# Performance work log

Measured on AMD Instinct MI355X. Metric: run time of the kernel, lower is better.

## Reference

```python
import jax, jax.numpy as jnp
import numpy as np

B1, B2, R, L, D, H = 48, 48, 36, 30, 1024, 4
EPS = 1e-8


def _l2norm(x):
    return x / (jnp.sqrt(jnp.sum(x * x, axis=-1, keepdims=True)) + EPS)


def _summary_attn(x, w1, b1, w2, b2):
    # x: (B1,B2,N,D). MLP scores -> softmax over N -> weighted mean over H heads.
    h = jax.nn.relu(jnp.einsum('abnd,ed->abne', x, w1) + b1)
    s = jnp.einsum('abne,he->abnh', h, w2) + b2          # (B1,B2,N,H)
    p = jax.nn.softmax(jnp.swapaxes(s, -1, -2), axis=-1)  # (B1,B2,H,N)
    w = jnp.einsum('abhn,abnd->abhd', p, x)               # (B1,B2,H,D)
    return w.mean(axis=-2)                                # (B1,B2,D)


def setup_inputs() -> dict:
    key = jax.random.key(0)
    ks = jax.random.split(key, 12)
    r = np.sqrt(6.0) / np.sqrt(D + D)  # xavier uniform as in init_weights
    return {
        'v1': jax.random.normal(ks[0], (B1, R, D), dtype=jnp.float32),
        'v2': jax.random.normal(ks[1], (B2, L, D), dtype=jnp.float32),
        'w_img': jax.random.uniform(ks[2], (D, D), jnp.float32, -r, r),
        'w_txt': jax.random.uniform(ks[3], (D, D), jnp.float32, -r, r),
        'w1a': jax.random.normal(ks[4], (D, D), jnp.float32) * 0.02,
        'b1a': jnp.zeros((D,), jnp.float32),
        'w2a': jax.random.normal(ks[5], (H, D), jnp.float32) * 0.02,
        'b2a': jnp.zeros((H,), jnp.float32),
        'w1b': jax.random.normal(ks[6], (D, D), jnp.float32) * 0.02,
        'b1b': jnp.zeros((D,), jnp.float32),
        'w2b': jax.random.normal(ks[7], (H, D), jnp.float32) * 0.02,
        'b2b': jnp.zeros((H,), jnp.float32),
    }


def reference(v1, v2, w_img, w_txt, w1a, b1a, w2a, b2a, w1b, b1b, w2b, b2b):
    d = v1.shape[-1]
    inv_sqrt_d = np.float32(1.0 / np.sqrt(d))
    k1 = jnp.einsum('ard,ed->are', v1, w_img)  # (B1,R,D)
    k2 = jnp.einsum('bld,ed->ble', v2, w_txt)  # (B2,L,D)

    # qkv_attention(k2, k1, v1): queries=words, keys/values=regions
    s1 = jnp.einsum('bld,ard->ablr', k2, k1) * inv_sqrt_d   # (B1,B2,L,R)
    p1 = jax.nn.softmax(s1, axis=-1)
    fused_v2 = jnp.einsum('ablr,ard->abld', p1, v1)         # weighted_v1 -> fused_v2

    # qkv_attention(k1, k2, v2): queries=regions, keys/values=words
    s2 = jnp.einsum('ard,bld->abrl', k1, k2) * inv_sqrt_d   # (B1,B2,R,L)
    p2 = jax.nn.softmax(s2, axis=-1)
    fused_v1 = jnp.einsum('abrl,bld->abrd', p2, v2)         # weighted_v2 -> fused_v1

    co_v1 = _l2norm(_summary_attn(fused_v1, w1a, b1a, w2a, b2a))
    co_v2 = _l2norm(_summary_attn(fused_v2, w1b, b1b, w2b, b2b))
    return jnp.sum(co_v1 * co_v2, axis=-1)  # (B1,B2) score matrix
```

## Files before the change

kernel.cpp:

```cpp
#include <hip/hip_runtime.h>

#define D 1024
#define NB1 48
#define NB2 48
#define RR 36
#define LL 30
#define NH 4

typedef short bf16x8 __attribute__((ext_vector_type(8)));
typedef float f32x4 __attribute__((ext_vector_type(4)));
typedef float f32x2 __attribute__((ext_vector_type(2)));
typedef unsigned short u16x8 __attribute__((ext_vector_type(8)));

#define MFMA16(a, b, c) __builtin_amdgcn_mfma_f32_16x16x32_bf16(a, b, c, 0, 0, 0)

__device__ __forceinline__ unsigned short f2bf(float x) {
  unsigned u = __float_as_uint(x);
  u += 0x7FFF + ((u >> 16) & 1);
  return (unsigned short)(u >> 16);
}
__device__ __forceinline__ float bf2f(unsigned short h) {
  return __uint_as_float(((unsigned)h) << 16);
}
__device__ __forceinline__ void split8(const float* v, bf16x8& h8, bf16x8& l8) {
  u16x8 hi, lo;
#pragma unroll
  for (int i = 0; i < 8; ++i) {
    unsigned short h = f2bf(v[i]);
    hi[i] = h;
    lo[i] = f2bf(v[i] - bf2f(h));
  }
  h8 = __builtin_bit_cast(bf16x8, hi);
  l8 = __builtin_bit_cast(bf16x8, lo);
}
__device__ __forceinline__ f32x2 shflx2(f32x2 v, int m) {
  double d = __builtin_bit_cast(double, v);
  d = __shfl_xor(d, m);
  return __builtin_bit_cast(f32x2, d);
}

__device__ __forceinline__ void conv_body(const float* __restrict__ X,
                                          unsigned short* __restrict__ out,
                                          int rows, int g) {
  const int lane = threadIdx.x & 63;
  const int tile = g >> 5, kc = g & 31;
  const int row = tile * 16 + (lane & 15);
  const int k = kc * 32 + (lane >> 4) * 8;
  float v[8];
  if (row < rows) {
    const float4* s = (const float4*)(X + (size_t)row * 1024 + k);
    float4 x0 = s[0], x1 = s[1];
    v[0] = x0.x; v[1] = x0.y; v[2] = x0.z; v[3] = x0.w;
    v[4] = x1.x; v[5] = x1.y; v[6] = x1.z; v[7] = x1.w;
  } else {
#pragma unroll
    for (int i = 0; i < 8; ++i) v[i] = 0.f;
  }
  bf16x8 hi, lo;
  split8(v, hi, lo);
  bf16x8* o = (bf16x8*)(out + (size_t)g * 1024 + lane * 8);
  o[0] = hi;
  o[64] = lo;
}

__global__ __launch_bounds__(256) void conv6(
    const float* __restrict__ v1, const float* __restrict__ v2,
    const float* __restrict__ wimg, const float* __restrict__ wtxt,
    const float* __restrict__ w1a, const float* __restrict__ w1b,
    unsigned short* v1f, unsigned short* v2f, unsigned short* wimgf,
    unsigned short* wtxtf, unsigned short* w1af, unsigned short* w1bf) {
  const float* X; unsigned short* O; int rows;
  switch (blockIdx.y) {
    case 0: X = v1; O = v1f; rows = 1728; break;
    case 1: X = v2; O = v2f; rows = 1440; break;
    case 2: X = wimg; O = wimgf; rows = 1024; break;
    case 3: X = wtxt; O = wtxtf; rows = 1024; break;
    case 4: X = w1a; O = w1af; rows = 1024; break;
    default: X = w1b; O = w1bf; rows = 1024; break;
  }
  const int tiles = (rows + 15) >> 4;
  const int g = blockIdx.x * 4 + (threadIdx.x >> 6);
  if (g >= tiles * 32) return;
  conv_body(X, O, rows, g);
}

__global__ __launch_bounds__(256) void conv_k(const float* __restrict__ k1,
                                              const float* __restrict__ k2,
                                              unsigned short* k1f, unsigned short* k2f) {
  const float* X = blockIdx.y ? k2 : k1;
  unsigned short* O = blockIdx.y ? k2f : k1f;
  const int rows = blockIdx.y ? 1440 : 1728;
  const int tiles = (rows + 15) >> 4;
  const int g = blockIdx.x * 4 + (threadIdx.x >> 6);
  if (g >= tiles * 32) return;
  conv_body(X, O, rows, g);
}

__global__ __launch_bounds__(256) void convG(const float* __restrict__ G2a,
                                             const float* __restrict__ G1b,
                                             const float* __restrict__ w2a,
                                             const float* __restrict__ w2b,
                                             unsigned short* G2aF, unsigned short* G1bF,
                                             float4* __restrict__ w2at,
                                             float4* __restrict__ w2bt) {
  const int t = threadIdx.x, lane = t & 63;
  if (blockIdx.y == 0 && blockIdx.x < 4) {
    int col = blockIdx.x * 256 + t;
    w2at[col] = make_float4(w2a[col], w2a[1024 + col], w2a[2048 + col], w2a[3072 + col]);
    w2bt[col] = make_float4(w2b[col], w2b[1024 + col], w2b[2048 + col], w2b[3072 + col]);
  }
  const int bb = blockIdx.x >> 4;
  const int nt = ((blockIdx.x & 15) << 2) + (t >> 6);
  const int c = lane & 15, q = lane >> 4;
  if (blockIdx.y == 0) {
    float v[8];
#pragma unroll
    for (int j = 0; j < 8; ++j) {
      int l = q * 8 + j;
      v[j] = (l < LL) ? G2a[(size_t)(bb * LL + l) * D + nt * 16 + c] : 0.f;
    }
    bf16x8 hi, lo;
    split8(v, hi, lo);
    bf16x8* o = (bf16x8*)(G2aF + ((size_t)(bb * 64 + nt) * 2) * 512 + lane * 8);
    o[0] = hi;
    o[64] = lo;
  } else {
#pragma unroll
    for (int kc = 0; kc < 2; ++kc) {
      float v[8];
#pragma unroll
      for (int j = 0; j < 8; ++j) {
        int r = kc * 32 + q * 8 + j;
        v[j] = (r < RR) ? G1b[(size_t)(bb * RR + r) * D + nt * 16 + c] : 0.f;
      }
      bf16x8 hi, lo;
      split8(v, hi, lo);
      bf16x8* o = (bf16x8*)(G1bF + (((size_t)(bb * 64 + nt) * 2 + kc) * 2) * 512 + lane * 8);
      o[0] = hi;
      o[64] = lo;
    }
  }
}

#define LOAD_FRAGS(AH, AL, BH, BL)                                              \
  {                                                                             \
    _Pragma("unroll") for (int i = 0; i < 4; ++i) {                             \
      AH[i] = Af[ab[i]]; AL[i] = Af[ab[i] + 64]; ab[i] += 128;                  \
    }                                                                           \
    _Pragma("unroll") for (int j = 0; j < 4; ++j) {                             \
      BH[j] = Bf[bb[j]]; BL[j] = Bf[bb[j] + 64]; bb[j] += 128;                  \
    }                                                                           \
  }

#define MFMA_SET(AH, AL, BH, BL)                                                \
  _Pragma("unroll") for (int i = 0; i < 4; ++i)                                 \
      _Pragma("unroll") for (int j = 0; j < 4; ++j) {                           \
    acc[i][j] = MFMA16(AH[i], BH[j], acc[i][j]);                                \
    acc[i][j] = MFMA16(AL[i], BH[j], acc[i][j]);                                \
    acc[i][j] = MFMA16(AH[i], BL[j], acc[i][j]);                                \
  }

__device__ __forceinline__ void gemm4_body(const bf16x8* __restrict__ Af,
                                           const bf16x8* __restrict__ Bf,
                                           float* __restrict__ C,
                                           int M, int N, float scale,
                                           int Mtiles, int Ntiles) {
  const int lane = threadIdx.x & 63;
  const int w = threadIdx.x >> 6;
  const int mb = blockIdx.y * 8 + (w >> 1) * 4;
  const int nb = blockIdx.x * 8 + (w & 1) * 4;
  int ab[4], bb[4];
#pragma unroll
  for (int i = 0; i < 4; ++i) {
    int tm = mb + i; if (tm > Mtiles - 1) tm = Mtiles - 1;
    ab[i] = tm * 4096 + lane;
    int tn = nb + i; if (tn > Ntiles - 1) tn = Ntiles - 1;
    bb[i] = tn * 4096 + lane;
  }
  f32x4 acc[4][4];
#pragma unroll
  for (int i = 0; i < 4; ++i)
#pragma unroll
    for (int j = 0; j < 4; ++j) acc[i][j] = (f32x4){0.f, 0.f, 0.f, 0.f};

  bf16x8 ahA[4], alA[4], bhA[4], blA[4];
  bf16x8 ahB[4], alB[4], bhB[4], blB[4];
  LOAD_FRAGS(ahA, alA, bhA, blA);
#pragma unroll 1
  for (int kc = 0; kc < 30; kc += 2) {
    LOAD_FRAGS(ahB, alB, bhB, blB);
    MFMA_SET(ahA, alA, bhA, blA);
    LOAD_FRAGS(ahA, alA, bhA, blA);
    MFMA_SET(ahB, alB, bhB, blB);
  }
  LOAD_FRAGS(ahB, alB, bhB, blB);
  MFMA_SET(ahA, alA, bhA, blA);
  MFMA_SET(ahB, alB, bhB, blB);

  const int c16 = lane & 15, q = lane >> 4;
#pragma unroll
  for (int i = 0; i < 4; ++i) {
#pragma unroll
    for (int reg = 0; reg < 4; ++reg) {
      int r = (mb + i) * 16 + q * 4 + reg;
      if (r < M) {
#pragma unroll
        for (int j = 0; j < 4; ++j) {
          int col = (nb + j) * 16 + c16;
          if (col < N) C[(size_t)r * N + col] = acc[i][j][reg] * scale;
        }
      }
    }
  }
}

__global__ __launch_bounds__(256) void proj_fused(
    const bf16x8* __restrict__ v1f, const bf16x8* __restrict__ v2f,
    const bf16x8* __restrict__ wimgf, const bf16x8* __restrict__ wtxtf,
    const bf16x8* __restrict__ w1af, const bf16x8* __restrict__ w1bf,
    float* k1, float* k2, float* G2a, float* G1b) {
  const int z = blockIdx.z;
  const bf16x8* Af = (z == 0 || z == 3) ? v1f : v2f;
  const bf16x8* Bf = (z == 0) ? wimgf : (z == 1) ? wtxtf : (z == 2) ? w1af : w1bf;
  float* C = (z == 0) ? k1 : (z == 1) ? k2 : (z == 2) ? G2a : G1b;
  const int M = (z == 0 || z == 3) ? 1728 : 1440;
  const int Mt = (z == 0 || z == 3) ? 108 : 92;
  if ((int)blockIdx.y * 8 >= Mt) return;
  gemm4_body(Af, Bf, C, M, 1024, 1.f, Mt, 64);
}

__global__ __launch_bounds__(256) void cross_s(
    const bf16x8* __restrict__ k2f, const bf16x8* __restrict__ k1f,
    float* Sbuf) {
  gemm4_body(k2f, k1f, Sbuf, 1440, 1728, 0.03125f, 92, 108);
}

__global__ __launch_bounds__(256, 4) void pair_dir(
    const float* __restrict__ Sb,
    const bf16x8* __restrict__ G2aF, const bf16x8* __restrict__ G1bF,
    const float* __restrict__ b1a, const float4* __restrict__ w2at, const float* __restrict__ b2a,
    const float* __restrict__ b1b, const float4* __restrict__ w2bt, const float* __restrict__ b2b,
    float* __restrict__ U1buf, float* __restrict__ U2buf) {
  const int t = threadIdx.x, lane = t & 63, w = t >> 6;
  const int id = blockIdx.x * 4 + w;
  const int pair = id >> 1, dir = id & 1;
  const int a = pair / NB2;
  const int b = pair - a * NB2;
  const int c16 = lane & 15, q = lane >> 4;

  union WSM {
    struct { float p2s[48][36]; float sa[48][NH]; float qa[48]; } A;
    struct { float p1s[32][68]; float sbm[32][NH]; float qb[32]; } B;
  };
  __shared__ __align__(16) WSM sm[4];
  WSM& S = sm[w];

  const float* Sab = Sb + (size_t)(b * LL) * 1728 + a * RR;

  if (dir == 0) {
    for (int i = lane; i < 48 * 36; i += 64) ((float*)S.A.p2s)[i] = 0.f;
    __builtin_amdgcn_sched_barrier(0);
    for (int i = lane; i < LL * RR; i += 64) {
      int l = i / RR, r = i - l * RR;
      S.A.p2s[r][l] = Sab[(size_t)l * 1728 + r];
    }
    __builtin_amdgcn_sched_barrier(0);
    if (lane < RR) {
      const int r = lane;
      float m = -1e30f;
      for (int l = 0; l < LL; ++l) m = fmaxf(m, S.A.p2s[r][l]);
      float s = 0.f;
      for (int l = 0; l < LL; ++l) {
        float e = __expf(S.A.p2s[r][l] - m);
        S.A.p2s[r][l] = e;
        s += e;
      }
      float inv = 1.f / s;
      for (int l = 0; l < LL; ++l) S.A.p2s[r][l] *= inv;
    }
    __builtin_amdgcn_sched_barrier(0);

    bf16x8 pAh[3], pAl[3];
#pragma unroll
    for (int mt = 0; mt < 3; ++mt) {
      float v[8];
      const float* rp = &S.A.p2s[mt * 16 + c16][q * 8];
      float4 x0 = *(const float4*)rp;
      float4 x1 = *(const float4*)(rp + 4);
      v[0] = x0.x; v[1] = x0.y; v[2] = x0.z; v[3] = x0.w;
      v[4] = x1.x; v[5] = x1.y; v[6] = x1.z; v[7] = x1.w;
      split8(v, pAh[mt], pAl[mt]);
    }

    f32x2 sc01[3][4], sc23[3][4];
#pragma unroll
    for (int mt = 0; mt < 3; ++mt)
#pragma unroll
      for (int reg = 0; reg < 4; ++reg) {
        sc01[mt][reg] = (f32x2){0.f, 0.f};
        sc23[mt][reg] = (f32x2){0.f, 0.f};
      }

    const bf16x8* gA = G2aF + (size_t)(b * 64) * 128 + lane;
#pragma unroll 2
    for (int it = 0; it < 64; ++it) {
      const bf16x8* gp = gA + (size_t)it * 128;
      bf16x8 Bh = gp[0], Bl = gp[64];
      const int col = it * 16 + c16;
      float4 wv = w2at[col];
      float bias = b1a[col];
      f32x2 w01 = {wv.x, wv.y}, w23 = {wv.z, wv.w};
#pragma unroll
      for (int mt = 0; mt < 3; ++mt) {
        f32x4 acc = {bias, bias, bias, bias};
        __builtin_amdgcn_s_setprio(1);
        acc = MFMA16(pAh[mt], Bh, acc);
        acc = MFMA16(pAl[mt], Bh, acc);
        acc = MFMA16(pAh[mt], Bl, acc);
        __builtin_amdgcn_s_setprio(0);
#pragma unroll
        for (int reg = 0; reg < 4; ++reg) {
          float hv = fmaxf(acc[reg], 0.f);
          f32x2 hv2 = {hv, hv};
          sc01[mt][reg] += hv2 * w01;
          sc23[mt][reg] += hv2 * w23;
        }
      }
    }
    f32x2 b01 = {b2a[0], b2a[1]}, b23 = {b2a[2], b2a[3]};
#pragma unroll
    for (int mt = 0; mt < 3; ++mt)
#pragma unroll
      for (int reg = 0; reg < 4; ++reg) {
        f32x2 v01 = sc01[mt][reg], v23 = sc23[mt][reg];
#pragma unroll
        for (int m = 1; m <= 8; m <<= 1) {
          v01 += shflx2(v01, m);
          v23 += shflx2(v23, m);
        }
        if (c16 == 0) {
          f32x2* rp = (f32x2*)&S.A.sa[mt * 16 + q * 4 + reg][0];
          rp[0] = v01 + b01;
          rp[1] = v23 + b23;
        }
      }
    __builtin_amdgcn_sched_barrier(0);
    {
      const int h = q, i = c16;
      float x0 = S.A.sa[i][h];
      float x1 = S.A.sa[i + 16][h];
      float x2 = (i < 4) ? S.A.sa[i + 32][h] : -1e30f;
      float m = fmaxf(fmaxf(x0, x1), x2);
      m = fmaxf(m, __shfl_xor(m, 1));
      m = fmaxf(m, __shfl_xor(m, 2));
      m = fmaxf(m, __shfl_xor(m, 4));
      m = fmaxf(m, __shfl_xor(m, 8));
      float e0 = __expf(x0 - m), e1 = __expf(x1 - m);
      float e2 = (i < 4) ? __expf(x2 - m) : 0.f;
      float s = e0 + e1 + e2;
      s += __shfl_xor(s, 1);
      s += __shfl_xor(s, 2);
      s += __shfl_xor(s, 4);
      s += __shfl_xor(s, 8);
      float inv = 0.25f / s;
      float p0 = e0 * inv, p1 = e1 * inv, p2v = e2 * inv;
      p0 += __shfl_xor(p0, 16); p0 += __shfl_xor(p0, 32);
      p1 += __shfl_xor(p1, 16); p1 += __shfl_xor(p1, 32);
      p2v += __shfl_xor(p2v, 16); p2v += __shfl_xor(p2v, 32);
      if (q == 0) {
        S.A.qa[i] = p0;
        S.A.qa[i + 16] = p1;
        if (i < 4) S.A.qa[i + 32] = p2v;
      }
    }
    __builtin_amdgcn_sched_barrier(0);
    if (lane < LL) {
      const int l = lane;
      float x = 0.f;
      for (int r = 0; r < RR; ++r) x = fmaf(S.A.qa[r], S.A.p2s[r][l], x);
      U2buf[((size_t)b * 48 + a) * 32 + l] = x;
    }
  } else {
    for (int i = lane; i < 32 * 68; i += 64) ((float*)S.B.p1s)[i] = 0.f;
    __builtin_amdgcn_sched_barrier(0);
    for (int i = lane; i < LL * RR; i += 64) {
      int l = i / RR, r = i - l * RR;
      S.B.p1s[l][r] = Sab[(size_t)l * 1728 + r];
    }
    __builtin_amdgcn_sched_barrier(0);
    if (lane < LL) {
      const int l = lane;
      float m = -1e30f;
      for (int r = 0; r < RR; ++r) m = fmaxf(m, S.B.p1s[l][r]);
      float s = 0.f;
      for (int r = 0; r < RR; ++r) {
        float e = __expf(S.B.p1s[l][r] - m);
        S.B.p1s[l][r] = e;
        s += e;
      }
      float inv = 1.f / s;
      for (int r = 0; r < RR; ++r) S.B.p1s[l][r] *= inv;
    }
    __builtin_amdgcn_sched_barrier(0);

    bf16x8 pBh[2][2], pBl[2][2];
#pragma unroll
    for (int mt = 0; mt < 2; ++mt)
#pragma unroll
      for (int kc = 0; kc < 2; ++kc) {
        float v[8];
        const float* rp = &S.B.p1s[mt * 16 + c16][kc * 32 + q * 8];
        float4 x0 = *(const float4*)rp;
        float4 x1 = *(const float4*)(rp + 4);
        v[0] = x0.x; v[1] = x0.y; v[2] = x0.z; v[3] = x0.w;
        v[4] = x1.x; v[5] = x1.y; v[6] = x1.z; v[7] = x1.w;
        split8(v, pBh[mt][kc], pBl[mt][kc]);
      }

    f32x2 sc01[2][4], sc23[2][4];
#pragma unroll
    for (int mt = 0; mt < 2; ++mt)
#pragma unroll
      for (int reg = 0; reg < 4; ++reg) {
        sc01[mt][reg] = (f32x2){0.f, 0.f};
        sc23[mt][reg] = (f32x2){0.f, 0.f};
      }

    const bf16x8* gB = G1bF + (size_t)(a * 64) * 256 + lane;
#pragma unroll 2
    for (int it = 0; it < 64; ++it) {
      const bf16x8* gp = gB + (size_t)it * 256;
      bf16x8 B0h = gp[0], B0l = gp[64], B1h = gp[128], B1l = gp[192];
      const int col = it * 16 + c16;
      float4 wv = w2bt[col];
      float bias = b1b[col];
      f32x2 w01 = {wv.x, wv.y}, w23 = {wv.z, wv.w};
#pragma unroll
      for (int mt = 0; mt < 2; ++mt) {
        f32x4 acc = {bias, bias, bias, bias};
        __builtin_amdgcn_s_setprio(1);
        acc = MFMA16(pBh[mt][0], B0h, acc);
        acc = MFMA16(pBl[mt][0], B0h, acc);
        acc = MFMA16(pBh[mt][0], B0l, acc);
        acc = MFMA16(pBh[mt][1], B1h, acc);
        acc = MFMA16(pBl[mt][1], B1h, acc);
        acc = MFMA16(pBh[mt][1], B1l, acc);
        __builtin_amdgcn_s_setprio(0);
#pragma unroll
        for (int reg = 0; reg < 4; ++reg) {
          float hv = fmaxf(acc[reg], 0.f);
          f32x2 hv2 = {hv, hv};
          sc01[mt][reg] += hv2 * w01;
          sc23[mt][reg] += hv2 * w23;
        }
      }
    }
    f32x2 b01 = {b2b[0], b2b[1]}, b23 = {b2b[2], b2b[3]};
#pragma unroll
    for (int mt = 0; mt < 2; ++mt)
#pragma unroll
      for (int reg = 0; reg < 4; ++reg) {
        f32x2 v01 = sc01[mt][reg], v23 = sc23[mt][reg];
#pragma unroll
        for (int m = 1; m <= 8; m <<= 1) {
          v01 += shflx2(v01, m);
          v23 += shflx2(v23, m);
        }
        if (c16 == 0) {
          f32x2* rp = (f32x2*)&S.B.sbm[mt * 16 + q * 4 + reg][0];
          rp[0] = v01 + b01;
          rp[1] = v23 + b23;
        }
      }
    __builtin_amdgcn_sched_barrier(0);
    {
      const int h = q, i = c16;
      float x0 = S.B.sbm[i][h];
      float x1 = (i < 14) ? S.B.sbm[i + 16][h] : -1e30f;
      float m = fmaxf(x0, x1);
      m = fmaxf(m, __shfl_xor(m, 1));
      m = fmaxf(m, __shfl_xor(m, 2));
      m = fmaxf(m, __shfl_xor(m, 4));
      m = fmaxf(m, __shfl_xor(m, 8));
      float e0 = __expf(x0 - m);
      float e1 = (i < 14) ? __expf(x1 - m) : 0.f;
      float s = e0 + e1;
      s += __shfl_xor(s, 1);
      s += __shfl_xor(s, 2);
      s += __shfl_xor(s, 4);
      s += __shfl_xor(s, 8);
      float inv = 0.25f / s;
      float p0 = e0 * inv, p1 = e1 * inv;
      p0 += __shfl_xor(p0, 16); p0 += __shfl_xor(p0, 32);
      p1 += __shfl_xor(p1, 16); p1 += __shfl_xor(p1, 32);
      if (q == 0) {
        S.B.qb[i] = p0;
        if (i < 14) S.B.qb[i + 16] = p1;
      }
    }
    __builtin_amdgcn_sched_barrier(0);
    if (lane < RR) {
      const int r = lane;
      float x = 0.f;
      for (int l = 0; l < LL; ++l) x = fmaf(S.B.qb[l], S.B.p1s[l][r], x);
      U1buf[((size_t)a * 48 + b) * 40 + r] = x;
    }
  }
}

__global__ __launch_bounds__(256) void y_batch(
    const float* __restrict__ v1, const float* __restrict__ v2,
    const float* __restrict__ U1buf, const float* __restrict__ U2buf,
    float* __restrict__ YA, float* __restrict__ YB) {
  const int bb = blockIdx.x;
  const int col = blockIdx.z * 256 + threadIdx.x;
  __shared__ float us[48 * 40];
  float y[48];
#pragma unroll
  for (int i = 0; i < 48; ++i) y[i] = 0.f;
  if (blockIdx.y == 0) {
    for (int i = threadIdx.x; i < 48 * 32; i += 256) us[i] = U2buf[(size_t)bb * 1536 + i];
    __syncthreads();
    const float* V = v2 + (size_t)bb * LL * 1024 + col;
    for (int l = 0; l < LL; ++l) {
      float v = V[(size_t)l * 1024];
#pragma unroll
      for (int i = 0; i < 48; ++i) y[i] = fmaf(us[i * 32 + l], v, y[i]);
    }
    float* Yo = YA + (size_t)bb * 48 * 1024 + col;
#pragma unroll
    for (int i = 0; i < 48; ++i) Yo[(size_t)i * 1024] = y[i];
  } else {
    for (int i = threadIdx.x; i < 48 * 40; i += 256) us[i] = U1buf[(size_t)bb * 1920 + i];
    __syncthreads();
    const float* V = v1 + (size_t)bb * RR * 1024 + col;
    for (int r = 0; r < RR; ++r) {
      float v = V[(size_t)r * 1024];
#pragma unroll
      for (int i = 0; i < 48; ++i) y[i] = fmaf(us[i * 40 + r], v, y[i]);
    }
    float* Yo = YB + (size_t)bb * 48 * 1024 + col;
#pragma unroll
    for (int i = 0; i < 48; ++i) Yo[(size_t)i * 1024] = y[i];
  }
}

__global__ __launch_bounds__(256) void pair_final(
    const float* __restrict__ YA, const float* __restrict__ YB,
    float* __restrict__ out) {
  const int pair = blockIdx.x;
  const int a = pair / NB2;
  const int b = pair - a * NB2;
  const int t = threadIdx.x;
  const float4* ya = (const float4*)(YA + ((size_t)b * 48 + a) * 1024);
  const float4* yb = (const float4*)(YB + ((size_t)a * 48 + b) * 1024);
  float4 va = ya[t], vb = yb[t];
  float num = va.x * vb.x + va.y * vb.y + va.z * vb.z + va.w * vb.w;
  float n1 = va.x * va.x + va.y * va.y + va.z * va.z + va.w * va.w;
  float n2 = vb.x * vb.x + vb.y * vb.y + vb.z * vb.z + vb.w * vb.w;
#pragma unroll
  for (int off = 32; off; off >>= 1) {
    num += __shfl_down(num, off);
    n1 += __shfl_down(n1, off);
    n2 += __shfl_down(n2, off);
  }
  __shared__ float r3[3][4];
  if ((t & 63) == 0) {
    r3[0][t >> 6] = num; r3[1][t >> 6] = n1; r3[2][t >> 6] = n2;
  }
  __syncthreads();
  if (t == 0) {
    float nu = r3[0][0] + r3[0][1] + r3[0][2] + r3[0][3];
    float s1 = sqrtf(fmaxf(r3[1][0] + r3[1][1] + r3[1][2] + r3[1][3], 0.f));
    float s2 = sqrtf(fmaxf(r3[2][0] + r3[2][1] + r3[2][2] + r3[2][3], 0.f));
    out[pair] = nu / ((s1 + 1e-8f) * (s2 + 1e-8f));
  }
}

extern "C" void kernel_launch(void* const* d_in, const int* in_sizes, int n_in,
                              void* d_out, int out_size, void* d_ws, size_t ws_size,
                              hipStream_t stream) {
  const float* v1    = (const float*)d_in[0];
  const float* v2    = (const float*)d_in[1];
  const float* w_img = (const float*)d_in[2];
  const float* w_txt = (const float*)d_in[3];
  const float* w1a   = (const float*)d_in[4];
  const float* b1a   = (const float*)d_in[5];
  const float* w2a   = (const float*)d_in[6];
  const float* b2a   = (const float*)d_in[7];
  const float* w1b   = (const float*)d_in[8];
  const float* b1b   = (const float*)d_in[9];
  const float* w2b   = (const float*)d_in[10];
  const float* b2b   = (const float*)d_in[11];
  float* out = (float*)d_out;

  float* ws   = (float*)d_ws;
  float* k1   = ws;
  float* k2   = k1 + (size_t)1728 * 1024;
  float* G2a  = k2 + (size_t)1440 * 1024;
  float* G1b  = G2a + (size_t)1440 * 1024;
  float* Sbuf = G1b + (size_t)1728 * 1024;
  float* Cbuf = Sbuf + (size_t)1440 * 1728;
  float* g22  = Cbuf + (size_t)1440 * 1728;
  float* g11  = g22 + (size_t)48 * 900;

  unsigned short* fb    = (unsigned short*)(g11 + (size_t)48 * 1296);
  unsigned short* v1f   = fb;
  unsigned short* v2f   = v1f + (size_t)108 * 32768;
  unsigned short* k1f   = v2f + (size_t)92 * 32768;
  unsigned short* k2f   = k1f + (size_t)108 * 32768;
  unsigned short* wimgf = k2f + (size_t)92 * 32768;
  unsigned short* wtxtf = wimgf + (size_t)64 * 32768;
  unsigned short* w1af  = wtxtf + (size_t)64 * 32768;
  unsigned short* w1bf  = w1af + (size_t)64 * 32768;
  unsigned short* G2aF  = w1bf + (size_t)64 * 32768;
  unsigned short* G1bF  = G2aF + (size_t)48 * 65536;

  float4* w2at = (float4*)k1;
  float4* w2bt = w2at + 1024;

  float* U2buf = G2a;
  float* U1buf = U2buf + (size_t)48 * 48 * 32;
  float* YA = Cbuf;
  float* YB = (float*)k1f;

  conv6<<<dim3(864, 6), 256, 0, stream>>>(v1, v2, w_img, w_txt, w1a, w1b,
                                          v1f, v2f, wimgf, wtxtf, w1af, w1bf);

  proj_fused<<<dim3(8, 14, 4), 256, 0, stream>>>(
      (const bf16x8*)v1f, (const bf16x8*)v2f, (const bf16x8*)wimgf,
      (const bf16x8*)wtxtf, (const bf16x8*)w1af, (const bf16x8*)w1bf,
      k1, k2, G2a, G1b);

  conv_k<<<dim3(864, 2), 256, 0, stream>>>(k1, k2, k1f, k2f);
  convG<<<dim3(768, 2), 256, 0, stream>>>(G2a, G1b, w2a, w2b, G2aF, G1bF, w2at, w2bt);

  cross_s<<<dim3(14, 12), 256, 0, stream>>>(
      (const bf16x8*)k2f, (const bf16x8*)k1f, Sbuf);

  pair_dir<<<1152, 256, 0, stream>>>(
      Sbuf, (const bf16x8*)G2aF, (const bf16x8*)G1bF,
      b1a, w2at, b2a, b1b, w2bt, b2b, U1buf, U2buf);
  y_batch<<<dim3(48, 2, 4), 256, 0, stream>>>(v1, v2, U1buf, U2buf, YA, YB);
  pair_final<<<2304, 256, 0, stream>>>(YA, YB, out);
}
```

Baseline: 295.6 us.

## Split pair attention into batched softmax, score GEMM, and small pair kernels

Replaces the per-pair pair_dir kernel with three stages. softmax_frag computes both softmaxes once per pair and writes bf16 hi/lo MFMA fragments. score_gemm batches all pairs sharing a G matrix into one large GEMM with the ReLU and head projection fused in. pair_small then does the final softmax over heads and the weighted reductions. It also merges conv_k and convG into one launch and switches the projection and cross GEMMs to 2-wave blocks with more blocks in the grid. The aim is better reuse of G fragments across pairs and better GPU occupancy, at the cost of extra intermediate buffers, extra launches, and recomputing exp in pair_small.

```diff
diff --git a/kernel.cpp b/kernel.cpp
--- a/kernel.cpp
+++ b/kernel.cpp
@@ -84,35 +84,35 @@
   conv_body(X, O, rows, g);
 }
 
-__global__ __launch_bounds__(256) void conv_k(const float* __restrict__ k1,
-                                              const float* __restrict__ k2,
-                                              unsigned short* k1f, unsigned short* k2f) {
-  const float* X = blockIdx.y ? k2 : k1;
-  unsigned short* O = blockIdx.y ? k2f : k1f;
-  const int rows = blockIdx.y ? 1440 : 1728;
-  const int tiles = (rows + 15) >> 4;
-  const int g = blockIdx.x * 4 + (threadIdx.x >> 6);
-  if (g >= tiles * 32) return;
-  conv_body(X, O, rows, g);
-}
-
-__global__ __launch_bounds__(256) void convG(const float* __restrict__ G2a,
-                                             const float* __restrict__ G1b,
-                                             const float* __restrict__ w2a,
-                                             const float* __restrict__ w2b,
-                                             unsigned short* G2aF, unsigned short* G1bF,
-                                             float4* __restrict__ w2at,
-                                             float4* __restrict__ w2bt) {
+__global__ __launch_bounds__(256) void convKG(
+    const float* __restrict__ k1, const float* __restrict__ k2,
+    const float* __restrict__ G2a, const float* __restrict__ G1b,
+    const float* __restrict__ w2a, const float* __restrict__ w2b,
+    unsigned short* k1f, unsigned short* k2f,
+    unsigned short* G2aF, unsigned short* G1bF,
+    float4* __restrict__ w2at, float4* __restrict__ w2bt) {
   const int t = threadIdx.x, lane = t & 63;
-  if (blockIdx.y == 0 && blockIdx.x < 4) {
+  const int y = blockIdx.y;
+  if (y < 2) {
+    const float* X = y ? k2 : k1;
+    unsigned short* O = y ? k2f : k1f;
+    const int rows = y ? 1440 : 1728;
+    const int tiles = (rows + 15) >> 4;
+    const int g = blockIdx.x * 4 + (t >> 6);
+    if (g >= tiles * 32) return;
+    conv_body(X, O, rows, g);
+    return;
+  }
+  if (y == 2 && blockIdx.x < 4) {
     int col = blockIdx.x * 256 + t;
     w2at[col] = make_float4(w2a[col], w2a[1024 + col], w2a[2048 + col], w2a[3072 + col]);
     w2bt[col] = make_float4(w2b[col], w2b[1024 + col], w2b[2048 + col], w2b[3072 + col]);
   }
+  if (blockIdx.x >= 768) return;
   const int bb = blockIdx.x >> 4;
   const int nt = ((blockIdx.x & 15) << 2) + (t >> 6);
   const int c = lane & 15, q = lane >> 4;
-  if (blockIdx.y == 0) {
+  if (y == 2) {
     float v[8];
 #pragma unroll
     for (int j = 0; j < 8; ++j) {
@@ -160,15 +160,15 @@
     acc[i][j] = MFMA16(AH[i], BL[j], acc[i][j]);                                \
   }
 
-__device__ __forceinline__ void gemm4_body(const bf16x8* __restrict__ Af,
-                                           const bf16x8* __restrict__ Bf,
-                                           float* __restrict__ C,
-                                           int M, int N, float scale,
-                                           int Mtiles, int Ntiles) {
+__device__ __forceinline__ void gemm2w_body(const bf16x8* __restrict__ Af,
+                                            const bf16x8* __restrict__ Bf,
+                                            float* __restrict__ C,
+                                            int M, int N, float scale,
+                                            int Mtiles, int Ntiles) {
   const int lane = threadIdx.x & 63;
   const int w = threadIdx.x >> 6;
-  const int mb = blockIdx.y * 8 + (w >> 1) * 4;
-  const int nb = blockIdx.x * 8 + (w & 1) * 4;
+  const int mb = blockIdx.y * 8 + w * 4;
+  const int nb = blockIdx.x * 4;
   int ab[4], bb[4];
 #pragma unroll
   for (int i = 0; i < 4; ++i) {
@@ -214,7 +214,7 @@
   }
 }
 
-__global__ __launch_bounds__(256) void proj_fused(
+__global__ __launch_bounds__(128) void proj_fused(
     const bf16x8* __restrict__ v1f, const bf16x8* __restrict__ v2f,
     const bf16x8* __restrict__ wimgf, const bf16x8* __restrict__ wtxtf,
     const bf16x8* __restrict__ w1af, const bf16x8* __restrict__ w1bf,
@@ -224,287 +224,284 @@
   const bf16x8* Bf = (z == 0) ? wimgf : (z == 1) ? wtxtf : (z == 2) ? w1af : w1bf;
   float* C = (z == 0) ? k1 : (z == 1) ? k2 : (z == 2) ? G2a : G1b;
   const int M = (z == 0 || z == 3) ? 1728 : 1440;
-  const int Mt = (z == 0 || z == 3) ? 108 : 92;
+  const int Mt = (z == 0 || z == 3) ? 108 : 90;
   if ((int)blockIdx.y * 8 >= Mt) return;
-  gemm4_body(Af, Bf, C, M, 1024, 1.f, Mt, 64);
-}
-
-__global__ __launch_bounds__(256) void cross_s(
+  gemm2w_body(Af, Bf, C, M, 1024, 1.f, Mt, 64);
+}
+
+__global__ __launch_bounds__(128) void cross_s(
     const bf16x8* __restrict__ k2f, const bf16x8* __restrict__ k1f,
     float* Sbuf) {
-  gemm4_body(k2f, k1f, Sbuf, 1440, 1728, 0.03125f, 92, 108);
-}
-
-__global__ __launch_bounds__(256, 4) void pair_dir(
-    const float* __restrict__ Sb,
-    const bf16x8* __restrict__ G2aF, const bf16x8* __restrict__ G1bF,
-    const float* __restrict__ b1a, const float4* __restrict__ w2at, const float* __restrict__ b2a,
-    const float* __restrict__ b1b, const float4* __restrict__ w2bt, const float* __restrict__ b2b,
-    float* __restrict__ U1buf, float* __restrict__ U2buf) {
+  gemm2w_body(k2f, k1f, Sbuf, 1440, 1728, 0.03125f, 90, 108);
+}
+
+__global__ __launch_bounds__(256) void softmax_frag(
+    const float* __restrict__ Sb, unsigned short* __restrict__ P2F,
+    unsigned short* __restrict__ P1F, float* __restrict__ MI) {
   const int t = threadIdx.x, lane = t & 63, w = t >> 6;
-  const int id = blockIdx.x * 4 + w;
-  const int pair = id >> 1, dir = id & 1;
-  const int a = pair / NB2;
-  const int b = pair - a * NB2;
+  const int pair = blockIdx.x * 4 + w;
+  const int a = pair / NB2, b = pair - a * NB2;
+  __shared__ __align__(16) float Sw_[4][30][36];
+  __shared__ float m2s_[4][36], i2s_[4][36], m1s_[4][30], i1s_[4][30];
+  float (*Sw)[36] = Sw_[w];
+  float* m2s = m2s_[w]; float* i2s = i2s_[w];
+  float* m1s = m1s_[w]; float* i1s = i1s_[w];
+  const float* Sab = Sb + (size_t)(b * LL) * 1728 + a * RR;
+  for (int i = lane; i < LL * RR; i += 64) {
+    int l = i / RR, r = i - l * RR;
+    Sw[l][r] = Sab[(size_t)l * 1728 + r];
+  }
+  __builtin_amdgcn_sched_barrier(0);
+  float* MIp = MI + (size_t)pair * 132;
+  if (lane < RR) {
+    const int r = lane;
+    float m = -1e30f;
+    for (int l = 0; l < LL; ++l) m = fmaxf(m, Sw[l][r]);
+    float s = 0.f;
+    for (int l = 0; l < LL; ++l) s += __expf(Sw[l][r] - m);
+    float inv = 1.f / s;
+    m2s[r] = m; i2s[r] = inv;
+    MIp[r] = m; MIp[36 + r] = inv;
+  }
+  if (lane < LL) {
+    const int l = lane;
+    float m = -1e30f;
+    for (int r = 0; r < RR; ++r) m = fmaxf(m, Sw[l][r]);
+    float s = 0.f;
+    for (int r = 0; r < RR; ++r) s += __expf(Sw[l][r] - m);
+    float inv = 1.f / s;
+    m1s[l] = m; i1s[l] = inv;
+    MIp[72 + l] = m; MIp[102 + l] = inv;
+  }
+  __builtin_amdgcn_sched_barrier(0);
+  for (int i = lane; i < 144; i += 64) {
+    int r = i >> 2, q = i & 3;
+    int rowg = a * RR + r, tt = rowg >> 4, c = rowg & 15;
+    float v[8];
+#pragma unroll
+    for (int j = 0; j < 8; ++j) {
+      int l = q * 8 + j;
+      v[j] = (l < LL) ? __expf(Sw[l][r] - m2s[r]) * i2s[r] : 0.f;
+    }
+    bf16x8 hi, lo;
+    split8(v, hi, lo);
+    bf16x8* o = (bf16x8*)(P2F + ((size_t)(b * 108 + tt) * 2) * 512 + (q * 16 + c) * 8);
+    o[0] = hi;
+    o[64] = lo;
+  }
+  for (int i = lane; i < 240; i += 64) {
+    int l = i >> 3, kq = i & 7, kc = kq >> 2, q = kq & 3;
+    int rowg = b * LL + l, tt = rowg >> 4, c = rowg & 15;
+    float v[8];
+#pragma unroll
+    for (int j = 0; j < 8; ++j) {
+      int r = kc * 32 + q * 8 + j;
+      v[j] = (r < RR) ? __expf(Sw[l][r] - m1s[l]) * i1s[l] : 0.f;
+    }
+    bf16x8 hi, lo;
+    split8(v, hi, lo);
+    bf16x8* o = (bf16x8*)(P1F + (((size_t)(a * 90 + tt) * 2 + kc) * 2) * 512 + (q * 16 + c) * 8);
+    o[0] = hi;
+    o[64] = lo;
+  }
+}
+
+__global__ __launch_bounds__(256) void score_gemm(
+    const bf16x8* __restrict__ P2Fv, const bf16x8* __restrict__ P1Fv,
+    const bf16x8* __restrict__ G2aFv, const bf16x8* __restrict__ G1bFv,
+    const float* __restrict__ b1a, const float4* __restrict__ w2at,
+    const float* __restrict__ b1b, const float4* __restrict__ w2bt,
+    float* __restrict__ SA, float* __restrict__ SB) {
+  const int t = threadIdx.x, lane = t & 63, w = t >> 6;
   const int c16 = lane & 15, q = lane >> 4;
-
-  union WSM {
-    struct { float p2s[48][36]; float sa[48][NH]; float qa[48]; } A;
-    struct { float p1s[32][68]; float sbm[32][NH]; float qb[32]; } B;
-  };
-  __shared__ __align__(16) WSM sm[4];
-  WSM& S = sm[w];
-
-  const float* Sab = Sb + (size_t)(b * LL) * 1728 + a * RR;
-
-  if (dir == 0) {
-    for (int i = lane; i < 48 * 36; i += 64) ((float*)S.A.p2s)[i] = 0.f;
-    __builtin_amdgcn_sched_barrier(0);
-    for (int i = lane; i < LL * RR; i += 64) {
-      int l = i / RR, r = i - l * RR;
-      S.A.p2s[r][l] = Sab[(size_t)l * 1728 + r];
-    }
-    __builtin_amdgcn_sched_barrier(0);
-    if (lane < RR) {
-      const int r = lane;
-      float m = -1e30f;
-      for (int l = 0; l < LL; ++l) m = fmaxf(m, S.A.p2s[r][l]);
-      float s = 0.f;
-      for (int l = 0; l < LL; ++l) {
-        float e = __expf(S.A.p2s[r][l] - m);
-        S.A.p2s[r][l] = e;
-        s += e;
-      }
-      float inv = 1.f / s;
-      for (int l = 0; l < LL; ++l) S.A.p2s[r][l] *= inv;
-    }
-    __builtin_amdgcn_sched_barrier(0);
-
-    bf16x8 pAh[3], pAl[3];
-#pragma unroll
-    for (int mt = 0; mt < 3; ++mt) {
-      float v[8];
-      const float* rp = &S.A.p2s[mt * 16 + c16][q * 8];
-      float4 x0 = *(const float4*)rp;
-      float4 x1 = *(const float4*)(rp + 4);
-      v[0] = x0.x; v[1] = x0.y; v[2] = x0.z; v[3] = x0.w;
-      v[4] = x1.x; v[5] = x1.y; v[6] = x1.z; v[7] = x1.w;
-      split8(v, pAh[mt], pAl[mt]);
-    }
-
-    f32x2 sc01[3][4], sc23[3][4];
-#pragma unroll
-    for (int mt = 0; mt < 3; ++mt)
-#pragma unroll
-      for (int reg = 0; reg < 4; ++reg) {
-        sc01[mt][reg] = (f32x2){0.f, 0.f};
-        sc23[mt][reg] = (f32x2){0.f, 0.f};
-      }
-
-    const bf16x8* gA = G2aF + (size_t)(b * 64) * 128 + lane;
+  const int x = blockIdx.x, bat = blockIdx.y;
+  __shared__ __align__(16) float red[4][64][4];
+  f32x2 sc01[4][4], sc23[4][4];
+#pragma unroll
+  for (int i = 0; i < 4; ++i)
+#pragma unroll
+    for (int reg = 0; reg < 4; ++reg) {
+      sc01[i][reg] = (f32x2){0.f, 0.f};
+      sc23[i][reg] = (f32x2){0.f, 0.f};
+    }
+
+  if (blockIdx.z == 0) {
+    const bf16x8* Pb = P2Fv + (size_t)bat * (108 * 128);
+    const bf16x8* Gb = G2aFv + (size_t)bat * (64 * 128);
+    bf16x8 aH[4], aL[4];
+#pragma unroll
+    for (int i = 0; i < 4; ++i) {
+      const bf16x8* pp = Pb + (size_t)(x * 4 + i) * 128 + lane;
+      aH[i] = pp[0];
+      aL[i] = pp[64];
+    }
 #pragma unroll 2
-    for (int it = 0; it < 64; ++it) {
-      const bf16x8* gp = gA + (size_t)it * 128;
+    for (int it = 0; it < 16; ++it) {
+      const int nt = w * 16 + it;
+      const bf16x8* gp = Gb + nt * 128 + lane;
       bf16x8 Bh = gp[0], Bl = gp[64];
-      const int col = it * 16 + c16;
+      const int col = nt * 16 + c16;
       float4 wv = w2at[col];
       float bias = b1a[col];
       f32x2 w01 = {wv.x, wv.y}, w23 = {wv.z, wv.w};
 #pragma unroll
-      for (int mt = 0; mt < 3; ++mt) {
+      for (int rt = 0; rt < 4; ++rt) {
         f32x4 acc = {bias, bias, bias, bias};
-        __builtin_amdgcn_s_setprio(1);
-        acc = MFMA16(pAh[mt], Bh, acc);
-        acc = MFMA16(pAl[mt], Bh, acc);
-        acc = MFMA16(pAh[mt], Bl, acc);
-        __builtin_amdgcn_s_setprio(0);
+        acc = MFMA16(aH[rt], Bh, acc);
+        acc = MFMA16(aL[rt], Bh, acc);
+        acc = MFMA16(aH[rt], Bl, acc);
 #pragma unroll
         for (int reg = 0; reg < 4; ++reg) {
           float hv = fmaxf(acc[reg], 0.f);
           f32x2 hv2 = {hv, hv};
-          sc01[mt][reg] += hv2 * w01;
-          sc23[mt][reg] += hv2 * w23;
+          sc01[rt][reg] += hv2 * w01;
+          sc23[rt][reg] += hv2 * w23;
         }
       }
     }
-    f32x2 b01 = {b2a[0], b2a[1]}, b23 = {b2a[2], b2a[3]};
-#pragma unroll
-    for (int mt = 0; mt < 3; ++mt)
-#pragma unroll
-      for (int reg = 0; reg < 4; ++reg) {
-        f32x2 v01 = sc01[mt][reg], v23 = sc23[mt][reg];
-#pragma unroll
-        for (int m = 1; m <= 8; m <<= 1) {
-          v01 += shflx2(v01, m);
-          v23 += shflx2(v23, m);
-        }
-        if (c16 == 0) {
-          f32x2* rp = (f32x2*)&S.A.sa[mt * 16 + q * 4 + reg][0];
-          rp[0] = v01 + b01;
-          rp[1] = v23 + b23;
-        }
+  } else {
+    if (x >= 23) return;
+    const bf16x8* Pa = P1Fv + (size_t)bat * (90 * 256);
+    const bf16x8* Ga = G1bFv + (size_t)bat * (64 * 256);
+    bf16x8 aH[4][2], aL[4][2];
+#pragma unroll
+    for (int i = 0; i < 4; ++i) {
+      int rtc = x * 4 + i; if (rtc > 89) rtc = 89;
+      const bf16x8* pp = Pa + (size_t)rtc * 256 + lane;
+#pragma unroll
+      for (int kc = 0; kc < 2; ++kc) {
+        aH[i][kc] = pp[kc * 128];
+        aL[i][kc] = pp[kc * 128 + 64];
       }
-    __builtin_amdgcn_sched_barrier(0);
-    {
-      const int h = q, i = c16;
-      float x0 = S.A.sa[i][h];
-      float x1 = S.A.sa[i + 16][h];
-      float x2 = (i < 4) ? S.A.sa[i + 32][h] : -1e30f;
-      float m = fmaxf(fmaxf(x0, x1), x2);
-      m = fmaxf(m, __shfl_xor(m, 1));
-      m = fmaxf(m, __shfl_xor(m, 2));
-      m = fmaxf(m, __shfl_xor(m, 4));
-      m = fmaxf(m, __shfl_xor(m, 8));
-      float e0 = __expf(x0 - m), e1 = __expf(x1 - m);
-      float e2 = (i < 4) ? __expf(x2 - m) : 0.f;
-      float s = e0 + e1 + e2;
-      s += __shfl_xor(s, 1);
-      s += __shfl_xor(s, 2);
-      s += __shfl_xor(s, 4);
-      s += __shfl_xor(s, 8);
-      float inv = 0.25f / s;
-      float p0 = e0 * inv, p1 = e1 * inv, p2v = e2 * inv;
-      p0 += __shfl_xor(p0, 16); p0 += __shfl_xor(p0, 32);
-      p1 += __shfl_xor(p1, 16); p1 += __shfl_xor(p1, 32);
-      p2v += __shfl_xor(p2v, 16); p2v += __shfl_xor(p2v, 32);
-      if (q == 0) {
-        S.A.qa[i] = p0;
-        S.A.qa[i + 16] = p1;
-        if (i < 4) S.A.qa[i + 32] = p2v;
-      }
-    }
-    __builtin_amdgcn_sched_barrier(0);
-    if (lane < LL) {
-      const int l = lane;
-      float x = 0.f;
-      for (int r = 0; r < RR; ++r) x = fmaf(S.A.qa[r], S.A.p2s[r][l], x);
-      U2buf[((size_t)b * 48 + a) * 32 + l] = x;
-    }
-  } else {
-    for (int i = lane; i < 32 * 68; i += 64) ((float*)S.B.p1s)[i] = 0.f;
-    __builtin_amdgcn_sched_barrier(0);
-    for (int i = lane; i < LL * RR; i += 64) {
-      int l = i / RR, r = i - l * RR;
-      S.B.p1s[l][r] = Sab[(size_t)l * 1728 + r];
-    }
-    __builtin_amdgcn_sched_barrier(0);
-    if (lane < LL) {
-      const int l = lane;
-      float m = -1e30f;
-      for (int r = 0; r < RR; ++r) m = fmaxf(m, S.B.p1s[l][r]);
-      float s = 0.f;
-      for (int r = 0; r < RR; ++r) {
-        float e = __expf(S.B.p1s[l][r] - m);
-        S.B.p1s[l][r] = e;
-        s += e;
-      }
-      float inv = 1.f / s;
-      for (int r = 0; r < RR; ++r) S.B.p1s[l][r] *= inv;
-    }
-    __builtin_amdgcn_sched_barrier(0);
-
-    bf16x8 pBh[2][2], pBl[2][2];
-#pragma unroll
-    for (int mt = 0; mt < 2; ++mt)
-#pragma unroll
-      for (int kc = 0; kc < 2; ++kc) {
-        float v[8];
-        const float* rp = &S.B.p1s[mt * 16 + c16][kc * 32 + q * 8];
-        float4 x0 = *(const float4*)rp;
-        float4 x1 = *(const float4*)(rp + 4);
-        v[0] = x0.x; v[1] = x0.y; v[2] = x0.z; v[3] = x0.w;
-        v[4] = x1.x; v[5] = x1.y; v[6] = x1.z; v[7] = x1.w;
-        split8(v, pBh[mt][kc], pBl[mt][kc]);
-      }
-
-    f32x2 sc01[2][4], sc23[2][4];
-#pragma unroll
-    for (int mt = 0; mt < 2; ++mt)
-#pragma unroll
-      for (int reg = 0; reg < 4; ++reg) {
-        sc01[mt][reg] = (f32x2){0.f, 0.f};
-        sc23[mt][reg] = (f32x2){0.f, 0.f};
-      }
-
-    const bf16x8* gB = G1bF + (size_t)(a * 64) * 256 + lane;
+    }
 #pragma unroll 2
-    for (int it = 0; it < 64; ++it) {
-      const bf16x8* gp = gB + (size_t)it * 256;
+    for (int it = 0; it < 16; ++it) {
+      const int nt = w * 16 + it;
+      const bf16x8* gp = Ga + nt * 256 + lane;
       bf16x8 B0h = gp[0], B0l = gp[64], B1h = gp[128], B1l = gp[192];
-      const int col = it * 16 + c16;
+      const int col = nt * 16 + c16;
       float4 wv = w2bt[col];
       float bias = b1b[col];
       f32x2 w01 = {wv.x, wv.y}, w23 = {wv.z, wv.w};
 #pragma unroll
-      for (int mt = 0; mt < 2; ++mt) {
+      for (int rt = 0; rt < 4; ++rt) {
         f32x4 acc = {bias, bias, bias, bias};
-        __builtin_amdgcn_s_setprio(1);
-        acc = MFMA16(pBh[mt][0], B0h, acc);
-        acc = MFMA16(pBl[mt][0], B0h, acc);
-        acc = MFMA16(pBh[mt][0], B0l, acc);
-        acc = MFMA16(pBh[mt][1], B1h, acc);
-        acc = MFMA16(pBl[mt][1], B1h, acc);
-        acc = MFMA16(pBh[mt][1], B1l, acc);
-        __builtin_amdgcn_s_setprio(0);
+        acc = MFMA16(aH[rt][0], B0h, acc);
+        acc = MFMA16(aL[rt][0], B0h, acc);
+        acc = MFMA16(aH[rt][0], B0l, acc);
+        acc = MFMA16(aH[rt][1], B1h, acc);
+        acc = MFMA16(aL[rt][1], B1h, acc);
+        acc = MFMA16(aH[rt][1], B1l, acc);
 #pragma unroll
         for (int reg = 0; reg < 4; ++reg) {
           float hv = fmaxf(acc[reg], 0.f);
           f32x2 hv2 = {hv, hv};
-          sc01[mt][reg] += hv2 * w01;
-          sc23[mt][reg] += hv2 * w23;
+          sc01[rt][reg] += hv2 * w01;
+          sc23[rt][reg] += hv2 * w23;
         }
       }
     }
-    f32x2 b01 = {b2b[0], b2b[1]}, b23 = {b2b[2], b2b[3]};
-#pragma unroll
-    for (int mt = 0; mt < 2; ++mt)
-#pragma unroll
-      for (int reg = 0; reg < 4; ++reg) {
-        f32x2 v01 = sc01[mt][reg], v23 = sc23[mt][reg];
-#pragma unroll
-        for (int m = 1; m <= 8; m <<= 1) {
-          v01 += shflx2(v01, m);
-          v23 += shflx2(v23, m);
-        }
-        if (c16 == 0) {
-          f32x2* rp = (f32x2*)&S.B.sbm[mt * 16 + q * 4 + reg][0];
-          rp[0] = v01 + b01;
-          rp[1] = v23 + b23;
-        }
+  }
+#pragma unroll
+  for (int rt = 0; rt < 4; ++rt)
+#pragma unroll
+    for (int reg = 0; reg < 4; ++reg) {
+      f32x2 v01 = sc01[rt][reg], v23 = sc23[rt][reg];
+#pragma unroll
+      for (int m = 1; m <= 8; m <<= 1) {
+        v01 += shflx2(v01, m);
+        v23 += shflx2(v23, m);
       }
-    __builtin_amdgcn_sched_barrier(0);
-    {
-      const int h = q, i = c16;
-      float x0 = S.B.sbm[i][h];
-      float x1 = (i < 14) ? S.B.sbm[i + 16][h] : -1e30f;
-      float m = fmaxf(x0, x1);
-      m = fmaxf(m, __shfl_xor(m, 1));
-      m = fmaxf(m, __shfl_xor(m, 2));
-      m = fmaxf(m, __shfl_xor(m, 4));
-      m = fmaxf(m, __shfl_xor(m, 8));
-      float e0 = __expf(x0 - m);
-      float e1 = (i < 14) ? __expf(x1 - m) : 0.f;
-      float s = e0 + e1;
-      s += __shfl_xor(s, 1);
-      s += __shfl_xor(s, 2);
-      s += __shfl_xor(s, 4);
-      s += __shfl_xor(s, 8);
-      float inv = 0.25f / s;
-      float p0 = e0 * inv, p1 = e1 * inv;
-      p0 += __shfl_xor(p0, 16); p0 += __shfl_xor(p0, 32);
-      p1 += __shfl_xor(p1, 16); p1 += __shfl_xor(p1, 32);
-      if (q == 0) {
-        S.B.qb[i] = p0;
-        if (i < 14) S.B.qb[i + 16] = p1;
+      if (c16 == 0) {
+        f32x2* rp = (f32x2*)&red[w][rt * 16 + q * 4 + reg][0];
+        rp[0] = v01;
+        rp[1] = v23;
       }
     }
-    __builtin_amdgcn_sched_barrier(0);
-    if (lane < RR) {
-      const int r = lane;
-      float x = 0.f;
-      for (int l = 0; l < LL; ++l) x = fmaf(S.B.qb[l], S.B.p1s[l][r], x);
-      U1buf[((size_t)a * 48 + b) * 40 + r] = x;
-    }
+  __syncthreads();
+  {
+    int row = t >> 2, h = t & 3;
+    float s = red[0][row][h] + red[1][row][h] + red[2][row][h] + red[3][row][h];
+    int rowg = x * 64 + row;
+    if (blockIdx.z == 0) {
+      SA[((size_t)bat * 1728 + rowg) * 4 + h] = s;
+    } else if (rowg < 1440) {
+      SB[((size_t)bat * 1440 + rowg) * 4 + h] = s;
+    }
+  }
+}
+
+__global__ __launch_bounds__(256) void pair_small(
+    const float* __restrict__ Sb, const float* __restrict__ SA,
+    const float* __restrict__ SB, const float* __restrict__ MI,
+    const float* __restrict__ b2a, const float* __restrict__ b2b,
+    float* __restrict__ U1buf, float* __restrict__ U2buf) {
+  const int t = threadIdx.x, lane = t & 63, w = t >> 6;
+  const int pair = blockIdx.x * 4 + w;
+  const int a = pair / NB2, b = pair - a * NB2;
+  __shared__ float qaS_[4][36], qbS_[4][30], m2S_[4][36], m1S_[4][30];
+  float* qaS = qaS_[w]; float* qbS = qbS_[w];
+  float* m2S = m2S_[w]; float* m1S = m1S_[w];
+  const float* MIp = MI + (size_t)pair * 132;
+
+  float4 sv = {0.f, 0.f, 0.f, 0.f};
+  if (lane < RR) {
+    sv = *(const float4*)&SA[((size_t)b * 1728 + a * RR + lane) * 4];
+    sv.x += b2a[0]; sv.y += b2a[1]; sv.z += b2a[2]; sv.w += b2a[3];
+  }
+  float qa = 0.f;
+#pragma unroll
+  for (int h = 0; h < 4; ++h) {
+    float xv = (lane < RR) ? ((float*)&sv)[h] : -1e30f;
+    float m = xv;
+#pragma unroll
+    for (int o = 1; o < 64; o <<= 1) m = fmaxf(m, __shfl_xor(m, o));
+    float ev = (lane < RR) ? __expf(xv - m) : 0.f;
+    float s = ev;
+#pragma unroll
+    for (int o = 1; o < 64; o <<= 1) s += __shfl_xor(s, o);
+    qa += ev / s;
+  }
+  if (lane < RR) {
+    qaS[lane] = 0.25f * qa * MIp[36 + lane];
+    m2S[lane] = MIp[lane];
+  }
+  float4 sw = {0.f, 0.f, 0.f, 0.f};
+  if (lane < LL) {
+    sw = *(const float4*)&SB[((size_t)a * 1440 + b * LL + lane) * 4];
+    sw.x += b2b[0]; sw.y += b2b[1]; sw.z += b2b[2]; sw.w += b2b[3];
+  }
+  float qb = 0.f;
+#pragma unroll
+  for (int h = 0; h < 4; ++h) {
+    float xv = (lane < LL) ? ((float*)&sw)[h] : -1e30f;
+    float m = xv;
+#pragma unroll
+    for (int o = 1; o < 64; o <<= 1) m = fmaxf(m, __shfl_xor(m, o));
+    float ev = (lane < LL) ? __expf(xv - m) : 0.f;
+    float s = ev;
+#pragma unroll
+    for (int o = 1; o < 64; o <<= 1) s += __shfl_xor(s, o);
+    qb += ev / s;
+  }
+  if (lane < LL) {
+    qbS[lane] = 0.25f * qb * MIp[102 + lane];
+    m1S[lane] = MIp[72 + lane];
+  }
+  __builtin_amdgcn_sched_barrier(0);
+
+  const float* Sab = Sb + (size_t)(b * LL) * 1728 + a * RR;
+  if (lane < LL) {
+    float xx = 0.f;
+    for (int r = 0; r < RR; ++r)
+      xx += qaS[r] * __expf(Sab[(size_t)lane * 1728 + r] - m2S[r]);
+    U2buf[((size_t)b * 48 + a) * 32 + lane] = xx;
+  }
+  if (lane < RR) {
+    float xx = 0.f;
+    for (int l = 0; l < LL; ++l)
+      xx += qbS[l] * __expf(Sab[(size_t)l * 1728 + lane] - m1S[l]);
+    U1buf[((size_t)a * 48 + b) * 40 + lane] = xx;
   }
 }
 
@@ -618,29 +615,39 @@
 
   float4* w2at = (float4*)k1;
   float4* w2bt = w2at + 1024;
-
-  float* U2buf = G2a;
+  float* SA = k2;
+  float* SB = SA + (size_t)48 * 1728 * 4;
+  float* MI = SB + (size_t)48 * 1440 * 4;
+  unsigned short* P2F = (unsigned short*)G2a;
+  unsigned short* P1F = v1f;
+  float* YA = Cbuf;
+  float* U2buf = Cbuf + (size_t)2304 * 1024;
   float* U1buf = U2buf + (size_t)48 * 48 * 32;
-  float* YA = Cbuf;
   float* YB = (float*)k1f;
 
   conv6<<<dim3(864, 6), 256, 0, stream>>>(v1, v2, w_img, w_txt, w1a, w1b,
                                           v1f, v2f, wimgf, wtxtf, w1af, w1bf);
 
-  proj_fused<<<dim3(8, 14, 4), 256, 0, stream>>>(
+  proj_fused<<<dim3(16, 14, 4), 128, 0, stream>>>(
       (const bf16x8*)v1f, (const bf16x8*)v2f, (const bf16x8*)wimgf,
       (const bf16x8*)wtxtf, (const bf16x8*)w1af, (const bf16x8*)w1bf,
       k1, k2, G2a, G1b);
 
-  conv_k<<<dim3(864, 2), 256, 0, stream>>>(k1, k2, k1f, k2f);
-  convG<<<dim3(768, 2), 256, 0, stream>>>(G2a, G1b, w2a, w2b, G2aF, G1bF, w2at, w2bt);
-
-  cross_s<<<dim3(14, 12), 256, 0, stream>>>(
+  convKG<<<dim3(864, 4), 256, 0, stream>>>(k1, k2, G2a, G1b, w2a, w2b,
+                                           k1f, k2f, G2aF, G1bF, w2at, w2bt);
+
+  cross_s<<<dim3(27, 12), 128, 0, stream>>>(
       (const bf16x8*)k2f, (const bf16x8*)k1f, Sbuf);
 
-  pair_dir<<<1152, 256, 0, stream>>>(
-      Sbuf, (const bf16x8*)G2aF, (const bf16x8*)G1bF,
-      b1a, w2at, b2a, b1b, w2bt, b2b, U1buf, U2buf);
+  softmax_frag<<<576, 256, 0, stream>>>(Sbuf, P2F, P1F, MI);
+
+  score_gemm<<<dim3(27, 48, 2), 256, 0, stream>>>(
+      (const bf16x8*)P2F, (const bf16x8*)P1F,
+      (const bf16x8*)G2aF, (const bf16x8*)G1bF,
+      b1a, w2at, b1b, w2bt, SA, SB);
+
+  pair_small<<<576, 256, 0, stream>>>(Sbuf, SA, SB, MI, b2a, b2b, U1buf, U2buf);
+
   y_batch<<<dim3(48, 2, 4), 256, 0, stream>>>(v1, v2, U1buf, U2buf, YA, YB);
   pair_final<<<2304, 256, 0, stream>>>(YA, YB, out);
 }
```

Result: slower. 317.6 us (+7.4%).

## Software-pipeline G-matrix loads in pair_dir and remap blocks for cache locality

Applied to the files above, without the earlier changes.

The 64-step loops over the G2a and G1b fragments in pair_dir now use a three-deep register rotation. The global loads for steps it+2 to it+4 are issued while the MFMA and ReLU-score work for the current step runs, which is meant to hide load latency. Block indexing is also remapped so that each block handles two adjacent b values for a single a, and consecutive blocks cycle through groups of 8 a values, to improve L2 reuse of the G fragments. The extra live fragment registers may push against the 4-waves-per-SIMD launch bound and cause spills.

```diff
diff --git a/kernel.cpp b/kernel.cpp
--- a/kernel.cpp
+++ b/kernel.cpp
@@ -242,10 +242,11 @@
     const float* __restrict__ b1b, const float4* __restrict__ w2bt, const float* __restrict__ b2b,
     float* __restrict__ U1buf, float* __restrict__ U2buf) {
   const int t = threadIdx.x, lane = t & 63, w = t >> 6;
-  const int id = blockIdx.x * 4 + w;
-  const int pair = id >> 1, dir = id & 1;
-  const int a = pair / NB2;
-  const int b = pair - a * NB2;
+  const int bx = blockIdx.x;
+  const int a = (bx & 7) + 8 * (bx / 192);
+  const int j = (bx >> 3) % 24;
+  const int b = j * 2 + (w >> 1);
+  const int dir = w & 1;
   const int c16 = lane & 15, q = lane >> 4;
 
   union WSM {
@@ -302,10 +303,12 @@
       }
 
     const bf16x8* gA = G2aF + (size_t)(b * 64) * 128 + lane;
-#pragma unroll 2
-    for (int it = 0; it < 64; ++it) {
+    auto loadA = [&](int it, bf16x8& Bh, bf16x8& Bl) {
       const bf16x8* gp = gA + (size_t)it * 128;
-      bf16x8 Bh = gp[0], Bl = gp[64];
+      Bh = gp[0];
+      Bl = gp[64];
+    };
+    auto compA = [&](bf16x8 Bh, bf16x8 Bl, int it) {
       const int col = it * 16 + c16;
       float4 wv = w2at[col];
       float bias = b1a[col];
@@ -326,6 +329,21 @@
           sc23[mt][reg] += hv2 * w23;
         }
       }
+    };
+    {
+      bf16x8 h0, l0, h1, l1, h2, l2;
+      loadA(0, h0, l0);
+      loadA(1, h1, l1);
+#pragma unroll 1
+      for (int it = 0; it < 63; it += 3) {
+        loadA(it + 2, h2, l2);
+        compA(h0, l0, it);
+        loadA(it + 3, h0, l0);
+        compA(h1, l1, it + 1);
+        loadA(it + 4 > 63 ? 63 : it + 4, h1, l1);
+        compA(h2, l2, it + 2);
+      }
+      compA(h0, l0, 63);
     }
     f32x2 b01 = {b2a[0], b2a[1]}, b23 = {b2a[2], b2a[3]};
 #pragma unroll
@@ -427,10 +445,14 @@
       }
 
     const bf16x8* gB = G1bF + (size_t)(a * 64) * 256 + lane;
-#pragma unroll 2
-    for (int it = 0; it < 64; ++it) {
+    auto loadB = [&](int it, bf16x8& B0h, bf16x8& B0l, bf16x8& B1h, bf16x8& B1l) {
       const bf16x8* gp = gB + (size_t)it * 256;
-      bf16x8 B0h = gp[0], B0l = gp[64], B1h = gp[128], B1l = gp[192];
+      B0h = gp[0];
+      B0l = gp[64];
+      B1h = gp[128];
+      B1l = gp[192];
+    };
+    auto compB = [&](bf16x8 B0h, bf16x8 B0l, bf16x8 B1h, bf16x8 B1l, int it) {
       const int col = it * 16 + c16;
       float4 wv = w2bt[col];
       float bias = b1b[col];
@@ -454,6 +476,21 @@
           sc23[mt][reg] += hv2 * w23;
         }
       }
+    };
+    {
+      bf16x8 a0, b0, c0, d0, a1, b1, c1, d1, a2, b2, c2, d2;
+      loadB(0, a0, b0, c0, d0);
+      loadB(1, a1, b1, c1, d1);
+#pragma unroll 1
+      for (int it = 0; it < 63; it += 3) {
+        loadB(it + 2, a2, b2, c2, d2);
+        compB(a0, b0, c0, d0, it);
+        loadB(it + 3, a0, b0, c0, d0);
+        compB(a1, b1, c1, d1, it + 1);
+        loadB(it + 4 > 63 ? 63 : it + 4, a1, b1, c1, d1);
+        compB(a2, b2, c2, d2, it + 2);
+      }
+      compB(a0, b0, c0, d0, 63);
     }
     f32x2 b01 = {b2b[0], b2b[1]}, b23 = {b2b[2], b2b[3]};
 #pragma unroll
```

Result: slower. 427.8 us (+44.7%).
